# Kernel tuning notes

Hardware: AMD Instinct MI355X
Metric: run time of the kernel (lower is better)

The kernel has to match this reference:

```python
import math
import jax, jax.numpy as jnp
import numpy as np

FACTOR = 5

def setup_inputs() -> dict:
    key = jax.random.key(0)
    k1, k2, k3, k4 = jax.random.split(key, 4)
    B, L, H, E = 4, 2048, 8, 64
    sample_k = min(L, max(1, int(FACTOR * math.ceil(math.log(L + 1)))))  # 40
    return {
        "queries": jax.random.normal(k1, (B, L, H, E), jnp.float32),
        "keys": jax.random.normal(k2, (B, L, H, E), jnp.float32),
        "values": jax.random.normal(k3, (B, L, H, E), jnp.float32),
        "index_sample": jax.random.randint(k4, (L, sample_k), 0, L),
    }

def reference(queries, keys, values, index_sample):
    # queries/keys/values: [B, L, H, E]; index_sample: [Lq, sample_k] int
    B, Lq, H, E = queries.shape
    Lk = keys.shape[1]
    q = jnp.transpose(queries, (0, 2, 1, 3))  # [B,H,Lq,E]
    k = jnp.transpose(keys, (0, 2, 1, 3))     # [B,H,Lk,E]
    v = jnp.transpose(values, (0, 2, 1, 3))   # [B,H,Lk,E]

    n_top = min(Lq, max(1, int(FACTOR * math.ceil(math.log(Lq + 1)))))
    scale = 1.0 / math.sqrt(E)

    # --- ProbSparse query scoring: sample keys per query, measure sparsity ---
    k_sample = k[:, :, index_sample, :]                       # [B,H,Lq,sk,E]
    qk_sample = jnp.einsum('bhle,bhlse->bhls', q, k_sample)   # [B,H,Lq,sk]
    sparsity = qk_sample.max(axis=-1) - qk_sample.mean(axis=-1)  # [B,H,Lq]
    _, top_idx = jax.lax.top_k(sparsity, n_top)               # [B,H,n_top]

    # --- Full scores only for the top queries ---
    q_top = jnp.take_along_axis(q, top_idx[..., None], axis=2)    # [B,H,n_top,E]
    scores = jnp.einsum('bhne,bhke->bhnk', q_top, k) * scale      # [B,H,n_top,Lk]

    # causal mask on the gathered rows (mask_flag=True, attn_mask=None)
    key_pos = jnp.arange(Lk)
    mask = key_pos[None, None, None, :] > top_idx[..., None]
    scores = jnp.where(mask, -jnp.inf, scores)
    attn = jax.nn.softmax(scores, axis=-1)                        # dropout = identity (eval)
    updates = jnp.einsum('bhnk,bhke->bhne', attn, v)              # [B,H,n_top,E]

    # --- cumsum-initialized context, scatter sparse rows back ---
    context = jnp.cumsum(v, axis=2)                               # [B,H,Lq,E]
    bi = jnp.arange(B)[:, None, None]
    hi = jnp.arange(H)[None, :, None]
    context = context.at[bi, hi, top_idx].set(updates)
    return jnp.transpose(context, (0, 2, 1, 3))                   # [B,Lq,H,E]
```

## Files before the change

### kernel.cpp

```cpp
#include <hip/hip_runtime.h>
#include <hip/hip_bf16.h>

#define BB 4
#define LL 2048
#define HH 8
#define EE 64
#define SK 40
#define NT 40
#define BH (BB*HH)
#define NCH 128
#define CLEN (LL/NCH)
#define KS 64
#define NS (LL/KS)
#define NQW 10

__device__ __forceinline__ size_t ro(int b, int l, int h) {
    return ((size_t)(b*LL + l)*HH + h)*EE;
}
__device__ __forceinline__ float bcast(float x, int sl) {
    return __uint_as_float(__builtin_amdgcn_readlane(__float_as_uint(x), sl));
}

__global__ __launch_bounds__(256) void k_spars(const float* __restrict__ q,
                                               const float* __restrict__ k,
                                               const int* __restrict__ samp,
                                               float* __restrict__ spars)
{
    __shared__ float pbuf[4][SK][20];
    int bid = blockIdx.x;
    int w    = threadIdx.x >> 6;
    int lane = threadIdx.x & 63;
    int bh = (((bid >> 3) & 3) << 3) | (bid & 7);
    int l  = (bid >> 5) * 4 + w;
    int b = bh >> 3, h = bh & 7;

    int sidx = (lane < SK) ? samp[l*SK + lane] : 0;

    const float4* qrow = (const float4*)(q + ro(b, l, h));
    float4 q4 = qrow[lane & 15];

    int sub = lane >> 4;
    #pragma unroll
    for (int g = 0; g < SK/4; ++g) {
        int s = 4*g + sub;
        int row = __shfl(sidx, s, 64);
        const float4* kr = (const float4*)(k + ro(b, row, h));
        float4 k4 = kr[lane & 15];
        float p = k4.x*q4.x + k4.y*q4.y + k4.z*q4.z + k4.w*q4.w;
        pbuf[w][s][lane & 15] = p;
    }
    float dot = 0.f;
    if (lane < SK) {
        const float4* pr = (const float4*)&pbuf[w][lane][0];
        float4 a = pr[0], b4 = pr[1], c4 = pr[2], d4 = pr[3];
        dot = ((a.x+a.y)+(a.z+a.w)) + ((b4.x+b4.y)+(b4.z+b4.w))
            + ((c4.x+c4.y)+(c4.z+c4.w)) + ((d4.x+d4.y)+(d4.z+d4.w));
    }
    float dmax = (lane < SK) ? dot : -INFINITY;
    float dsum = (lane < SK) ? dot : 0.f;
    #pragma unroll
    for (int off = 32; off; off >>= 1) {
        dmax = fmaxf(dmax, __shfl_xor(dmax, off, 64));
        dsum += __shfl_xor(dsum, off, 64);
    }
    if (lane == 0) spars[bh*LL + l] = dmax - dsum * (1.0f/SK);
}

__global__ __launch_bounds__(256) void k_topk(const float* __restrict__ spars,
                                              int* __restrict__ topidx,
                                              signed char* __restrict__ sel)
{
    __shared__ float wv[4];
    __shared__ int   wi[4];
    __shared__ int   top[NT];
    int bh = blockIdx.x, t = threadIdx.x, w = t >> 6, lane = t & 63;

    float r[8];
    #pragma unroll
    for (int i = 0; i < 8; ++i) r[i] = spars[bh*LL + i*256 + t];

    for (int n = 0; n < NT; ++n) {
        float bv = r[0]; int bi = t;
        #pragma unroll
        for (int i = 1; i < 8; ++i)
            if (r[i] > bv) { bv = r[i]; bi = i*256 + t; }
        #pragma unroll
        for (int off = 32; off; off >>= 1) {
            float ov = __shfl_xor(bv, off, 64);
            int   oi = __shfl_xor(bi, off, 64);
            if (ov > bv || (ov == bv && oi < bi)) { bv = ov; bi = oi; }
        }
        if (lane == 0) { wv[w] = bv; wi[w] = bi; }
        __syncthreads();
        float gv = wv[0]; int gi = wi[0];
        #pragma unroll
        for (int j = 1; j < 4; ++j) {
            float ov = wv[j]; int oi = wi[j];
            if (ov > gv || (ov == gv && oi < gi)) { gv = ov; gi = oi; }
        }
        if (t == 0) { top[n] = gi; topidx[bh*NT + n] = gi; }
        if ((gi & 255) == t) {
            int slot = gi >> 8;
            #pragma unroll
            for (int i = 0; i < 8; ++i) if (i == slot) r[i] = -INFINITY;
        }
        __syncthreads();
    }

    for (int l2 = t; l2 < LL; l2 += 256) sel[bh*LL + l2] = -1;
    __syncthreads();
    if (t < NT) sel[bh*LL + top[t]] = (signed char)t;
}

__global__ __launch_bounds__(256) void k_attn_split(const float* __restrict__ q,
                                                    const float* __restrict__ k,
                                                    const float* __restrict__ v,
                                                    const int* __restrict__ topidx,
                                                    float* __restrict__ pm,
                                                    float* __restrict__ pl,
                                                    __hip_bfloat16* __restrict__ pO)
{
    __shared__ float KT[EE][KS+1];
    __shared__ float Vs[KS][EE];
    __shared__ int   tix[NT];
    int bh = blockIdx.x >> 5, split = blockIdx.x & 31;
    int b = bh >> 3, h = bh & 7;
    int base = split * KS;
    int t = threadIdx.x, w = t >> 6, lane = t & 63;

    if (t < NT) tix[t] = topidx[bh*NT + t];
    __syncthreads();

    int rr = t >> 4, c4 = t & 15;
    #pragma unroll
    for (int p = 0; p < 4; ++p) {
        int kr = p*16 + rr;
        const float4* krow = (const float4*)(k + ro(b, base + kr, h));
        float4 x = krow[c4];
        KT[c4*4+0][kr] = x.x; KT[c4*4+1][kr] = x.y;
        KT[c4*4+2][kr] = x.z; KT[c4*4+3][kr] = x.w;
        const float4* vrow = (const float4*)(v + ro(b, base + kr, h));
        ((float4*)&Vs[kr][0])[c4] = vrow[c4];
    }

    float qreg[NQW]; int jn[NQW];
    #pragma unroll
    for (int r = 0; r < NQW; ++r) {
        int ti = tix[w*NQW + r];
        jn[r] = min(KS, ti - base + 1);
        qreg[r] = q[ro(b, ti, h) + lane] * 0.125f;
    }
    __syncthreads();

    float S[NQW];
    #pragma unroll
    for (int r = 0; r < NQW; ++r) S[r] = 0.f;
    for (int e0 = 0; e0 < EE; e0 += 16) {
        #pragma unroll
        for (int j = 0; j < 16; ++j) {
            int e = e0 + j;
            float ke = KT[e][lane];
            #pragma unroll
            for (int r = 0; r < NQW; ++r)
                S[r] = fmaf(ke, bcast(qreg[r], e), S[r]);
        }
    }

    float P[NQW], mloc[NQW], lloc[NQW];
    #pragma unroll
    for (int r = 0; r < NQW; ++r) {
        float s = (lane < jn[r]) ? S[r] : -INFINITY;
        float m = s;
        #pragma unroll
        for (int off = 32; off; off >>= 1) m = fmaxf(m, __shfl_xor(m, off, 64));
        bool act = jn[r] > 0;
        float p = act ? __expf(s - m) : 0.f;
        float ls = p;
        #pragma unroll
        for (int off = 32; off; off >>= 1) ls += __shfl_xor(ls, off, 64);
        P[r] = p; mloc[r] = act ? m : -INFINITY; lloc[r] = act ? ls : 0.f;
    }

    float O[NQW];
    #pragma unroll
    for (int r = 0; r < NQW; ++r) O[r] = 0.f;
    for (int k0 = 0; k0 < KS; k0 += 16) {
        #pragma unroll
        for (int j = 0; j < 16; ++j) {
            int kk = k0 + j;
            float ve = Vs[kk][lane];
            #pragma unroll
            for (int r = 0; r < NQW; ++r)
                O[r] = fmaf(ve, bcast(P[r], kk), O[r]);
        }
    }

    #pragma unroll
    for (int r = 0; r < NQW; ++r) {
        int n = w*NQW + r;
        size_t idx = (size_t)(bh*NT + n)*NS + split;
        if (lane == 0) { pm[idx] = mloc[r]; pl[idx] = lloc[r]; }
        pO[idx*EE + lane] = __float2bfloat16(O[r]);
    }
}

__global__ __launch_bounds__(256) void k_attn_comb(const float* __restrict__ pm,
                                                   const float* __restrict__ pl,
                                                   const __hip_bfloat16* __restrict__ pO,
                                                   float* __restrict__ upd)
{
    int wid  = (blockIdx.x * blockDim.x + threadIdx.x) >> 6;
    int lane = threadIdx.x & 63;
    float pmv = (lane < NS) ? pm[(size_t)wid*NS + lane] : -INFINITY;
    float plv = (lane < NS) ? pl[(size_t)wid*NS + lane] : 0.f;
    float M = pmv;
    #pragma unroll
    for (int off = 32; off; off >>= 1) M = fmaxf(M, __shfl_xor(M, off, 64));
    float sc = (lane < NS && pmv > -INFINITY) ? __expf(pmv - M) : 0.f;
    float L = plv * sc;
    #pragma unroll
    for (int off = 32; off; off >>= 1) L += __shfl_xor(L, off, 64);
    float O = 0.f;
    for (int s = 0; s < NS; ++s) {
        float w = bcast(sc, s);
        O += __bfloat162float(pO[((size_t)wid*NS + s)*EE + lane]) * w;
    }
    upd[(size_t)wid*EE + lane] = O / L;
}

__global__ __launch_bounds__(256) void k_csum(const float* __restrict__ v,
                                              float* __restrict__ csum)
{
    int wid  = (blockIdx.x * blockDim.x + threadIdx.x) >> 6;
    int lane = threadIdx.x & 63;
    int bh = wid / NCH, c = wid - bh*NCH;
    int b = bh >> 3, h = bh & 7;
    int l0 = c * CLEN;
    float s = 0.f;
    #pragma unroll 4
    for (int i = 0; i < CLEN; ++i)
        s += v[ro(b, l0 + i, h) + lane];
    csum[(size_t)wid*EE + lane] = s;
}

__global__ __launch_bounds__(256) void k_pfx(float* __restrict__ csum)
{
    __shared__ float buf[NCH*EE];
    __shared__ float gs[4*EE];
    int bh = blockIdx.x, t = threadIdx.x;
    int e = t & 63, g = t >> 6;

    for (int i = t; i < NCH*EE; i += 256) buf[i] = csum[(size_t)bh*NCH*EE + i];
    __syncthreads();

    float s = 0.f;
    for (int c = g*32; c < g*32+32; ++c) s += buf[c*EE + e];
    gs[g*EE + e] = s;
    __syncthreads();

    float run = 0.f;
    for (int j = 0; j < g; ++j) run += gs[j*EE + e];
    for (int c = g*32; c < g*32+32; ++c) {
        float x = buf[c*EE + e];
        buf[c*EE + e] = run;
        run += x;
    }
    __syncthreads();

    for (int i = t; i < NCH*EE; i += 256) csum[(size_t)bh*NCH*EE + i] = buf[i];
}

__global__ __launch_bounds__(256) void k_out(const float* __restrict__ v,
                                             const float* __restrict__ csum,
                                             const signed char* __restrict__ sel,
                                             const float* __restrict__ upd,
                                             float* __restrict__ out)
{
    int wid  = (blockIdx.x * blockDim.x + threadIdx.x) >> 6;
    int lane = threadIdx.x & 63;
    int bh = wid / NCH, c = wid - bh*NCH;
    int b = bh >> 3, h = bh & 7;

    float run = csum[((size_t)bh*NCH + c)*EE + lane];
    int l0 = c * CLEN;
    #pragma unroll 4
    for (int i = 0; i < CLEN; ++i) {
        int l = l0 + i;
        run += v[ro(b, l, h) + lane];
        int sn = sel[bh*LL + l];
        float val = (sn >= 0) ? upd[((size_t)bh*NT + sn)*EE + lane] : run;
        out[ro(b, l, h) + lane] = val;
    }
}

__global__ __launch_bounds__(256) void k_attn_old(const float* __restrict__ q,
                                                  const float* __restrict__ k,
                                                  const float* __restrict__ v,
                                                  const int* __restrict__ topidx,
                                                  float* __restrict__ upd)
{
    __shared__ float sc[LL];
    __shared__ float red[256];
    __shared__ float part[4][EE];
    int bh = blockIdx.x / NT, n = blockIdx.x % NT;
    int b = bh >> 3, h = bh & 7;
    int ti = topidx[bh*NT + n];
    int t = threadIdx.x, w = t >> 6, lane = t & 63;

    float qe = q[ro(b, ti, h) + lane];
    for (int j = w; j <= ti; j += 4) {
        float kv = k[ro(b, j, h) + lane];
        float p = qe * kv;
        #pragma unroll
        for (int off = 32; off; off >>= 1) p += __shfl_xor(p, off, 64);
        if (lane == 0) sc[j] = p * 0.125f;
    }
    __syncthreads();
    float m = -1e30f;
    for (int j = t; j <= ti; j += 256) m = fmaxf(m, sc[j]);
    red[t] = m; __syncthreads();
    for (int s2 = 128; s2; s2 >>= 1) { if (t < s2) red[t] = fmaxf(red[t], red[t+s2]); __syncthreads(); }
    m = red[0]; __syncthreads();
    float ssum = 0.f;
    for (int j = t; j <= ti; j += 256) { float p = __expf(sc[j] - m); sc[j] = p; ssum += p; }
    red[t] = ssum; __syncthreads();
    for (int s2 = 128; s2; s2 >>= 1) { if (t < s2) red[t] += red[t+s2]; __syncthreads(); }
    float inv = 1.0f / red[0];
    float acc = 0.f;
    for (int j = w; j <= ti; j += 4) acc += sc[j] * v[ro(b, j, h) + lane];
    part[w][lane] = acc;
    __syncthreads();
    if (w == 0) {
        float r = (part[0][lane] + part[1][lane] + part[2][lane] + part[3][lane]) * inv;
        upd[((size_t)bh*NT + n)*EE + lane] = r;
    }
}

extern "C" void kernel_launch(void* const* d_in, const int* in_sizes, int n_in,
                              void* d_out, int out_size, void* d_ws, size_t ws_size,
                              hipStream_t stream) {
    const float* q = (const float*)d_in[0];
    const float* k = (const float*)d_in[1];
    const float* v = (const float*)d_in[2];
    const int* samp = (const int*)d_in[3];
    float* out = (float*)d_out;

    char* ws = (char*)d_ws;
    float*          spars  = (float*)(ws);
    float*          pm     = (float*)(ws);
    int*            topidx = (int*)  (ws + 262144);
    signed char*    sel    = (signed char*)(ws + 262144 + 8192);
    float*          upd    = (float*)(ws + 262144 + 8192 + 65536);
    float*          pl     = (float*)(ws + 262144 + 8192 + 65536 + 327680);
    char*           pObase =          ws + 262144 + 8192 + 65536 + 327680 + 163840;
    __hip_bfloat16* pO     = (__hip_bfloat16*)pObase;
    float*          csum   = (float*)pObase;
    size_t full_need = 262144 + 8192 + 65536 + 327680 + 163840 + (size_t)BH*NT*NS*EE*2;

    k_spars<<<BH*LL/4, 256, 0, stream>>>(q, k, samp, spars);
    k_topk <<<BH,      256, 0, stream>>>(spars, topidx, sel);
    if (ws_size >= full_need) {
        k_attn_split<<<BH*NS, 256, 0, stream>>>(q, k, v, topidx, pm, pl, pO);
        k_attn_comb <<<BH*NT/4, 256, 0, stream>>>(pm, pl, pO, upd);
    } else {
        k_attn_old<<<BH*NT, 256, 0, stream>>>(q, k, v, topidx, upd);
    }
    k_csum<<<BH*NCH/4, 256, 0, stream>>>(v, csum);
    k_pfx <<<BH,       256, 0, stream>>>(csum);
    k_out <<<BH*NCH/4, 256, 0, stream>>>(v, csum, sel, upd, out);
}
```

Measured before the change: 217.4 us.

## Vectorize sparsity, chunk-sum and output kernels with float4 and shuffle reductions

The sparsity kernel drops its shared-memory staging buffer and reduces each dot product with wave shuffles, then tracks max and sum per 16-lane group. The chunk-sum kernel now has each wave read four rows at once with float4 loads and combine them with shuffles. The output kernel has each wave handle four chunks with float4 loads and stores, which cuts its wave count by four. The aim is fewer memory instructions and no LDS round trips, at the cost of less parallelism in k_out and a longer serial chain per lane.

```diff
diff --git a/kernel.cpp b/kernel.cpp
--- a/kernel.cpp
+++ b/kernel.cpp
@@ -26,44 +26,35 @@
                                                const int* __restrict__ samp,
                                                float* __restrict__ spars)
 {
-    __shared__ float pbuf[4][SK][20];
     int bid = blockIdx.x;
     int w    = threadIdx.x >> 6;
     int lane = threadIdx.x & 63;
     int bh = (((bid >> 3) & 3) << 3) | (bid & 7);
     int l  = (bid >> 5) * 4 + w;
     int b = bh >> 3, h = bh & 7;
+    int c = lane & 15, g = lane >> 4;
 
     int sidx = (lane < SK) ? samp[l*SK + lane] : 0;
-
-    const float4* qrow = (const float4*)(q + ro(b, l, h));
-    float4 q4 = qrow[lane & 15];
-
-    int sub = lane >> 4;
-    #pragma unroll
-    for (int g = 0; g < SK/4; ++g) {
-        int s = 4*g + sub;
+    const float4 q4 = ((const float4*)(q + ro(b, l, h)))[c];
+    const float* kbase = k + ((size_t)b*LL*HH + h)*EE;
+
+    float m = -INFINITY, ssum = 0.f;
+    #pragma unroll
+    for (int i = 0; i < SK/4; ++i) {
+        int s = 4*i + g;
         int row = __shfl(sidx, s, 64);
-        const float4* kr = (const float4*)(k + ro(b, row, h));
-        float4 k4 = kr[lane & 15];
+        float4 k4 = ((const float4*)(kbase + (size_t)row*(HH*EE)))[c];
         float p = k4.x*q4.x + k4.y*q4.y + k4.z*q4.z + k4.w*q4.w;
-        pbuf[w][s][lane & 15] = p;
-    }
-    float dot = 0.f;
-    if (lane < SK) {
-        const float4* pr = (const float4*)&pbuf[w][lane][0];
-        float4 a = pr[0], b4 = pr[1], c4 = pr[2], d4 = pr[3];
-        dot = ((a.x+a.y)+(a.z+a.w)) + ((b4.x+b4.y)+(b4.z+b4.w))
-            + ((c4.x+c4.y)+(c4.z+c4.w)) + ((d4.x+d4.y)+(d4.z+d4.w));
-    }
-    float dmax = (lane < SK) ? dot : -INFINITY;
-    float dsum = (lane < SK) ? dot : 0.f;
-    #pragma unroll
-    for (int off = 32; off; off >>= 1) {
-        dmax = fmaxf(dmax, __shfl_xor(dmax, off, 64));
-        dsum += __shfl_xor(dsum, off, 64);
-    }
-    if (lane == 0) spars[bh*LL + l] = dmax - dsum * (1.0f/SK);
+        #pragma unroll
+        for (int off = 1; off <= 8; off <<= 1) p += __shfl_xor(p, off, 64);
+        m = fmaxf(m, p);
+        ssum += p;
+    }
+    m = fmaxf(m, __shfl_xor(m, 16, 64));
+    m = fmaxf(m, __shfl_xor(m, 32, 64));
+    ssum += __shfl_xor(ssum, 16, 64);
+    ssum += __shfl_xor(ssum, 32, 64);
+    if (lane == 0) spars[bh*LL + l] = m - ssum * (1.0f/SK);
 }
 
 __global__ __launch_bounds__(256) void k_topk(const float* __restrict__ spars,
@@ -233,14 +224,24 @@
 {
     int wid  = (blockIdx.x * blockDim.x + threadIdx.x) >> 6;
     int lane = threadIdx.x & 63;
-    int bh = wid / NCH, c = wid - bh*NCH;
-    int b = bh >> 3, h = bh & 7;
-    int l0 = c * CLEN;
-    float s = 0.f;
-    #pragma unroll 4
-    for (int i = 0; i < CLEN; ++i)
-        s += v[ro(b, l0 + i, h) + lane];
-    csum[(size_t)wid*EE + lane] = s;
+    int bh = wid / NCH, cch = wid - bh*NCH;
+    int b = bh >> 3, h = bh & 7;
+    int r2 = lane >> 4, c4 = lane & 15;
+    int l0 = cch * CLEN;
+    float4 s4 = {0.f, 0.f, 0.f, 0.f};
+    #pragma unroll
+    for (int i = 0; i < CLEN/4; ++i) {
+        float4 x = ((const float4*)(v + ro(b, l0 + i*4 + r2, h)))[c4];
+        s4.x += x.x; s4.y += x.y; s4.z += x.z; s4.w += x.w;
+    }
+    #pragma unroll
+    for (int off = 16; off <= 32; off <<= 1) {
+        s4.x += __shfl_xor(s4.x, off, 64);
+        s4.y += __shfl_xor(s4.y, off, 64);
+        s4.z += __shfl_xor(s4.z, off, 64);
+        s4.w += __shfl_xor(s4.w, off, 64);
+    }
+    if (r2 == 0) ((float4*)(csum + ((size_t)bh*NCH + cch)*EE))[c4] = s4;
 }
 
 __global__ __launch_bounds__(256) void k_pfx(float* __restrict__ csum)
@@ -278,18 +279,21 @@
 {
     int wid  = (blockIdx.x * blockDim.x + threadIdx.x) >> 6;
     int lane = threadIdx.x & 63;
-    int bh = wid / NCH, c = wid - bh*NCH;
-    int b = bh >> 3, h = bh & 7;
-
-    float run = csum[((size_t)bh*NCH + c)*EE + lane];
-    int l0 = c * CLEN;
-    #pragma unroll 4
+    int bh = wid / (NCH/4), wc = wid - bh*(NCH/4);
+    int b = bh >> 3, h = bh & 7;
+    int g = lane >> 4, c4 = lane & 15;
+    int cch = wc*4 + g;
+    int l0 = cch * CLEN;
+
+    float4 run = ((const float4*)(csum + ((size_t)bh*NCH + cch)*EE))[c4];
     for (int i = 0; i < CLEN; ++i) {
         int l = l0 + i;
-        run += v[ro(b, l, h) + lane];
+        float4 x = ((const float4*)(v + ro(b, l, h)))[c4];
+        run.x += x.x; run.y += x.y; run.z += x.z; run.w += x.w;
         int sn = sel[bh*LL + l];
-        float val = (sn >= 0) ? upd[((size_t)bh*NT + sn)*EE + lane] : run;
-        out[ro(b, l, h) + lane] = val;
+        float4 o = run;
+        if (sn >= 0) o = ((const float4*)(upd + ((size_t)bh*NT + sn)*EE))[c4];
+        ((float4*)(out + ro(b, l, h)))[c4] = o;
     }
 }
 
@@ -365,7 +369,7 @@
     } else {
         k_attn_old<<<BH*NT, 256, 0, stream>>>(q, k, v, topidx, upd);
     }
-    k_csum<<<BH*NCH/4, 256, 0, stream>>>(v, csum);
-    k_pfx <<<BH,       256, 0, stream>>>(csum);
-    k_out <<<BH*NCH/4, 256, 0, stream>>>(v, csum, sel, upd, out);
-}
+    k_csum<<<BH*NCH/4,  256, 0, stream>>>(v, csum);
+    k_pfx <<<BH,        256, 0, stream>>>(csum);
+    k_out <<<BH*NCH/16, 256, 0, stream>>>(v, csum, sel, upd, out);
+}
```

Result: no change. 218.5 us (+0.5%).
